# Optimization experiments

Hardware: AMD Instinct MI355X
Metric: run time of the kernel (lower is better)

The kernel has to match this reference:

```python
import jax, jax.numpy as jnp
import numpy as np

B, L1, L2, H = 8, 384, 384, 128


def _lin(k, out_f, in_f, scale=0.05):
    kw, kb = jax.random.split(k)
    return (jax.random.normal(kw, (out_f, in_f), jnp.float32) * scale,
            jax.random.normal(kb, (out_f,), jnp.float32) * scale)


def setup_inputs() -> dict:
    key = jax.random.key(0)
    ks = jax.random.split(key, 10)
    Wq_w, Wq_b = _lin(ks[2], H, H)
    Wup_w, Wup_b = _lin(ks[3], H, H)
    Wvp_w, Wvp_b = _lin(ks[4], H, H)
    V_w, V_b = _lin(ks[5], 1, H)
    Wg_w, Wg_b = _lin(ks[6], 2 * H, 2 * H)
    W_ih, b_ih = _lin(ks[7], 4 * H, 2 * H)
    W_hh, b_hh = _lin(ks[8], 4 * H, H)
    return {
        "x": jax.random.normal(ks[0], (B, L1, H), jnp.float32),
        "x_mask": jnp.zeros((B, L1), dtype=bool),
        "y": jax.random.normal(ks[1], (B, L2, H), jnp.float32),
        "y_mask": jnp.zeros((B, L2), dtype=bool),
        "Wq_w": Wq_w, "Wq_b": Wq_b,
        "Wup_w": Wup_w, "Wup_b": Wup_b,
        "Wvp_w": Wvp_w, "Wvp_b": Wvp_b,
        "V_w": V_w, "V_b": V_b,
        "Wg_w": Wg_w, "Wg_b": Wg_b,
        "W_ih": W_ih, "W_hh": W_hh, "b_ih": b_ih, "b_hh": b_hh,
    }


def reference(x, x_mask, y, y_mask, Wq_w, Wq_b, Wup_w, Wup_b, Wvp_w, Wvp_b,
              V_w, V_b, Wg_w, Wg_b, W_ih, W_hh, b_ih, b_hh):
    b, l1, h = x.shape
    # projections (torch Linear: x @ W.T + b)
    x_proj = x @ Wup_w.T + Wup_b                      # [B, L1, H]
    y_proj = y @ Wq_w.T + Wq_b                        # [B, L2, H]
    # source feeds a constant zero hidden state into W_vp -> just its bias
    hidden_proj = jnp.zeros((h,), x.dtype) @ Wvp_w.T + Wvp_b  # [H]
    # additive attention scores: V . tanh(xp + yp + hp)
    sum_batch = jnp.tanh(x_proj[:, :, None, :] + y_proj[:, None, :, :] + hidden_proj)  # [B,L1,L2,H]
    s = jnp.einsum('btjh,h->btj', sum_batch, V_w[0]) + V_b[0]  # [B, L1, L2]
    # sum_mask = (1 - x_mask) outer (1 - y_mask)
    xm = 1.0 - x_mask.astype(s.dtype)
    ym = 1.0 - y_mask.astype(s.dtype)
    s = s * (xm[:, :, None] * ym[:, None, :])
    s = jnp.where(y_mask[:, None, :], -jnp.inf, s)
    alpha = jax.nn.softmax(s, axis=-1)                # [B, L1, L2]
    ct = jnp.einsum('btj,bjh->bth', alpha, y)         # [B, L1, H]
    merge = jnp.concatenate([x, ct], axis=2)          # [B, L1, 2H]
    gt = jax.nn.sigmoid(merge @ Wg_w.T + Wg_b)
    lstm_in = gt * merge                              # [B, L1, 2H]
    # single-layer unidirectional LSTM (torch gate order: i, f, g, o)
    gates_x = lstm_in @ W_ih.T + b_ih                 # [B, L1, 4H]

    def step(carry, gx):
        h_t, c_t = carry
        g = gx + h_t @ W_hh.T + b_hh
        i, f, gg, o = jnp.split(g, 4, axis=-1)
        c_n = jax.nn.sigmoid(f) * c_t + jax.nn.sigmoid(i) * jnp.tanh(gg)
        h_n = jax.nn.sigmoid(o) * jnp.tanh(c_n)
        return (h_n, c_n), h_n

    init = (jnp.zeros((b, h), x.dtype), jnp.zeros((b, h), x.dtype))
    _, hs = jax.lax.scan(step, init, jnp.swapaxes(gates_x, 0, 1))  # [L1, B, H]
    return jnp.swapaxes(hs, 0, 1)                     # [B, L1, H]
```

## Files before the change

kernel.cpp:

```cpp
#include <hip/hip_runtime.h>
#include <hip/hip_bf16.h>
#include <math.h>

typedef __attribute__((ext_vector_type(4))) float  float4v;
typedef __attribute__((ext_vector_type(2))) float  float2v;
typedef __attribute__((ext_vector_type(8))) short  short8;

#define B_ 8
#define L_ 384
#define H_ 128

__device__ __forceinline__ float bflo(unsigned int u){ unsigned int t = u << 16; float f; __builtin_memcpy(&f,&t,4); return f; }
__device__ __forceinline__ unsigned short f2bf(float f){
  unsigned int t; __builtin_memcpy(&t,&f,4);
  return (unsigned short)((t + 0x7fffu + ((t>>16)&1u)) >> 16);
}
__device__ __forceinline__ float fsig(float x){ return __fdividef(1.f, 1.f + __expf(-x)); }

__device__ __forceinline__ void barrier_lds(){
  asm volatile("s_waitcnt lgkmcnt(0)\n\ts_barrier" ::: "memory");
}

template<int K>
__device__ __forceinline__ void mfma_rowgemm_body(
    unsigned short* in_s,
    const float* __restrict__ inA,
    const float* __restrict__ W, const float* __restrict__ bias,
    const float* __restrict__ bias2, float* __restrict__ out,
    int Ntotal, int act, int row0, int ob)
{
  constexpr int KP = K + 2;
  const int tid  = threadIdx.x;
  const int w    = tid >> 6;
  const int l    = tid & 63;
  const int c    = l & 15;
  const int quad = l >> 4;

  #pragma unroll
  for (int it = 0; it < K/32; ++it) {
    int idx = it*256 + tid;
    int r = idx / (K/4);
    int k = (idx % (K/4)) * 4;
    float4v f = *(const float4v*)(inA + (size_t)(row0+r)*K + k);
    unsigned int p0 = (unsigned int)f2bf(f.x) | ((unsigned int)f2bf(f.y) << 16);
    unsigned int p1 = (unsigned int)f2bf(f.z) | ((unsigned int)f2bf(f.w) << 16);
    *(unsigned int*)&in_s[r*KP + k]     = p0;
    *(unsigned int*)&in_s[r*KP + k + 2] = p1;
  }

  const int n = ob + w*16 + c;
  short8 bfr[K/32];
  #pragma unroll
  for (int kt = 0; kt < K/32; ++kt) {
    const float* src = W + (size_t)n*K + kt*32 + quad*8;
    float4v f0 = *(const float4v*)(src);
    float4v f1 = *(const float4v*)(src + 4);
    short8 v;
    v[0]=(short)f2bf(f0[0]); v[1]=(short)f2bf(f0[1]); v[2]=(short)f2bf(f0[2]); v[3]=(short)f2bf(f0[3]);
    v[4]=(short)f2bf(f1[0]); v[5]=(short)f2bf(f1[1]); v[6]=(short)f2bf(f1[2]); v[7]=(short)f2bf(f1[3]);
    bfr[kt] = v;
  }
  __syncthreads();

  const float4v z4 = {0.f,0.f,0.f,0.f};
  float4v acc0 = z4, acc1 = z4;
  #pragma unroll
  for (int kt = 0; kt < K/32; ++kt) {
    short8 a0 = *(const short8*)&in_s[(c     )*KP + kt*32 + quad*8];
    short8 a1 = *(const short8*)&in_s[(16 + c)*KP + kt*32 + quad*8];
    acc0 = __builtin_amdgcn_mfma_f32_16x16x32_bf16(a0, bfr[kt], acc0, 0,0,0);
    acc1 = __builtin_amdgcn_mfma_f32_16x16x32_bf16(a1, bfr[kt], acc1, 0,0,0);
  }

  const float C2 = 2.8853900817779268f;
  float bv = bias[n] + (bias2 ? bias2[n] : 0.f);
  #pragma unroll
  for (int mt = 0; mt < 2; ++mt) {
    float4v A = mt ? acc1 : acc0;
    #pragma unroll
    for (int r = 0; r < 4; ++r) {
      int m = mt*16 + quad*4 + r;
      float val = A[r] + bv;
      if (act == 4)
        val = __builtin_amdgcn_exp2f(C2 * val);
      if (act == 3)
        out[(size_t)(row0+m)*Ntotal + (n & 127)*4 + (n >> 7)] = val;
      else
        out[(size_t)(row0+m)*Ntotal + n] = val;
    }
  }
}

template<int K>
__global__ __launch_bounds__(256) void mfma_rowgemm_kernel(
    const float* __restrict__ inA,
    const float* __restrict__ W, const float* __restrict__ bias,
    const float* __restrict__ bias2, float* __restrict__ out,
    int Ntotal, int act)
{
  __shared__ __align__(16) unsigned short in_s[32*(K+2)];
  mfma_rowgemm_body<K>(in_s, inA, W, bias, bias2, out,
                       Ntotal, act, blockIdx.x*32, blockIdx.y*64);
}

__global__ __launch_bounds__(256) void proj_mfma_kernel(
    const float* __restrict__ x, const float* __restrict__ y,
    const float* __restrict__ Wup_w, const float* __restrict__ Wup_b,
    const float* __restrict__ Wq_w, const float* __restrict__ Wq_b,
    const float* __restrict__ Wvp_b,
    float* __restrict__ xp, float* __restrict__ yp)
{
  __shared__ __align__(16) unsigned short in_s[32*130];
  int bx = blockIdx.x;
  if (bx < 192)
    mfma_rowgemm_body<128>(in_s, x, Wup_w, Wup_b, nullptr,
                           xp, 128, 4, (bx>>1)*32, (bx&1)*64);
  else {
    bx -= 192;
    mfma_rowgemm_body<128>(in_s, y, Wq_w, Wq_b, Wvp_b,
                           yp, 128, 4, (bx>>1)*32, (bx&1)*64);
  }
}

__global__ __launch_bounds__(256) void attn_kernel(
    const float* __restrict__ xp, const float* __restrict__ yp,
    const float* __restrict__ y, const unsigned char* __restrict__ xmask,
    const unsigned char* __restrict__ ymask, const float* __restrict__ Vw,
    const float* __restrict__ Vb,
    float* __restrict__ ctpbase, float* __restrict__ ml)
{
  __shared__ __align__(16) float xp_s[8][128];
  __shared__ __align__(16) float v2_s[128];
  __shared__ __align__(16) float yp_s[32][132];
  __shared__ __align__(16) unsigned short p_s[16][40];
  __shared__ float sc_s[16];
  __shared__ float xm_s[8];
  __shared__ float ym_s[32];
  __shared__ float sv_s;
  const int tid = threadIdx.x;
  const int b   = blockIdx.y;
  const int t0  = blockIdx.x * 8;
  const int jh  = blockIdx.z;
  const int jb  = jh * 96;
  const int w    = tid >> 6;
  const int l    = tid & 63;
  const int c16  = l & 15;
  const int quad = l >> 4;
  {
    int r = tid >> 5, k4 = (tid & 31) * 4;
    float4v f = *(const float4v*)(xp + ((size_t)(b*L_ + t0 + r))*H_ + k4);
    *(float4v*)&xp_s[r][k4] = f;
    if (tid < 32) {
      float4v v = *(const float4v*)(Vw + tid*4);
      float4v v2; v2[0]=2.f*v[0]; v2[1]=2.f*v[1]; v2[2]=2.f*v[2]; v2[3]=2.f*v[3];
      *(float4v*)&v2_s[tid*4] = v2;
    }
    if (tid < 8) xm_s[tid] = xmask[b*L_ + t0 + tid] ? 0.f : 1.f;
    if (tid < 16) sc_s[tid] = 0.f;
    for (int i = 320 + tid; i < 640; i += 256) ((unsigned short*)p_s)[i] = 0;
  }
  __syncthreads();
  if (tid < 32) {
    float4v v = *(const float4v*)&v2_s[tid*4];
    float sm = (v[0]+v[1]) + (v[2]+v[3]);
    #pragma unroll
    for (int off = 16; off >= 1; off >>= 1) sm += __shfl_xor(sm, off);
    if (tid == 0) sv_s = 0.5f*sm + Vb[0];
  }

  float4v rp[4];
  unsigned char ymb = 0;
  {
    #pragma unroll
    for (int it = 0; it < 4; ++it) {
      int idx = it*256 + tid; int r = idx >> 5; int k4 = (idx & 31) * 4;
      rp[it] = *(const float4v*)(yp + ((size_t)(b*L_ + jb + r))*H_ + k4);
    }
    if (tid < 32) ymb = ymask[b*L_ + jb + tid];
  }

  const int t = tid >> 5, u = tid & 31;
  float mrun = -__builtin_inff(), lrun = 0.f;
  const float4v z4 = {0.f,0.f,0.f,0.f};
  float4v acc0 = z4, acc1 = z4;
  float svc = 0.f, xmv = 0.f;

  for (int c = 0; c < 3; ++c) {
    __syncthreads();
    #pragma unroll
    for (int it = 0; it < 4; ++it) {
      int idx = it*256 + tid; int r = idx >> 5; int k4 = (idx & 31) * 4;
      *(float4v*)&yp_s[r][k4] = rp[it];
    }
    if (tid < 32) ym_s[tid] = ymb ? 0.f : 1.f;
    __syncthreads();
    if (c == 0) { svc = sv_s; xmv = xm_s[t]; }
    short8 yb0, yb1;
    {
      const float* ybase = y + ((size_t)(b*L_ + jb + c*32 + quad*8))*H_ + c16;
      #pragma unroll
      for (int jj = 0; jj < 8; ++jj) {
        yb0[jj] = (short)f2bf(ybase[(size_t)jj*H_ + w*16]);
        yb1[jj] = (short)f2bf(ybase[(size_t)jj*H_ + (w+4)*16]);
      }
    }
    if (c < 2) {
      #pragma unroll
      for (int it = 0; it < 4; ++it) {
        int idx = it*256 + tid; int r = idx >> 5; int k4 = (idx & 31) * 4;
        rp[it] = *(const float4v*)(yp + ((size_t)(b*L_ + jb + (c+1)*32 + r))*H_ + k4);
      }
      if (tid < 32) ymb = ymask[b*L_ + jb + (c+1)*32 + tid];
    }

    float sA = 0.f, sB = 0.f;
    {
      const float* yr = yp_s[u];
      const float* xr = xp_s[t];
      #pragma unroll 4
      for (int k = 0; k < 128; k += 4) {
        float4v yv = *(const float4v*)&yr[k];
        float4v xv = *(const float4v*)&xr[k];
        float4v vv = *(const float4v*)&v2_s[k];
        sA -= vv[0] * __builtin_amdgcn_rcpf(__builtin_fmaf(xv[0], yv[0], 1.f));
        sB -= vv[1] * __builtin_amdgcn_rcpf(__builtin_fmaf(xv[1], yv[1], 1.f));
        sA -= vv[2] * __builtin_amdgcn_rcpf(__builtin_fmaf(xv[2], yv[2], 1.f));
        sB -= vv[3] * __builtin_amdgcn_rcpf(__builtin_fmaf(xv[3], yv[3], 1.f));
      }
    }
    float ymv = ym_s[u];
    float s = (svc + sA + sB) * xmv * ymv;
    if (ymv == 0.f) s = -__builtin_inff();
    float mc = s;
    #pragma unroll
    for (int off = 16; off >= 1; off >>= 1) mc = fmaxf(mc, __shfl_xor(mc, off));
    float mnew = fmaxf(mrun, mc);
    float p  = __expf(s - mnew);
    float sc = __expf(mrun - mnew);
    float ps = p;
    #pragma unroll
    for (int off = 16; off >= 1; off >>= 1) ps += __shfl_xor(ps, off);
    lrun = lrun * sc + ps;
    mrun = mnew;
    p_s[t][u] = f2bf(p);
    if (u == 0) sc_s[t] = sc;
    __syncthreads();
    short8 pf = *(const short8*)&p_s[c16][quad*8];
    float4v scv;
    #pragma unroll
    for (int r = 0; r < 4; ++r) scv[r] = sc_s[quad*4 + r];
    acc0 *= scv; acc1 *= scv;
    acc0 = __builtin_amdgcn_mfma_f32_16x16x32_bf16(pf, yb0, acc0, 0,0,0);
    acc1 = __builtin_amdgcn_mfma_f32_16x16x32_bf16(pf, yb1, acc1, 0,0,0);
  }
  float* ctp = ctpbase + (size_t)jh*393216;
  if (quad < 2) {
    #pragma unroll
    for (int r = 0; r < 4; ++r) {
      int row = b*L_ + t0 + quad*4 + r;
      ctp[(size_t)row*H_ + w*16 + c16]     = acc0[r];
      ctp[(size_t)row*H_ + (w+4)*16 + c16] = acc1[r];
    }
  }
  if (u == 0) {
    int row = b*L_ + t0 + t;
    ml[(jh*2+0)*3072 + row] = mrun;
    ml[(jh*2+1)*3072 + row] = lrun;
  }
}

__global__ __launch_bounds__(256) void gate1_kernel(
    const float* __restrict__ x,
    const float* __restrict__ ctpbase, const float* __restrict__ ml,
    const float* __restrict__ Wg_w, const float* __restrict__ Wg_b,
    float* __restrict__ out)
{
  constexpr int K = 256, KP = 258;
  __shared__ __align__(16) unsigned short in_s[32*KP];
  const int tid  = threadIdx.x;
  const int w    = tid >> 6;
  const int l    = tid & 63;
  const int c    = l & 15;
  const int quad = l >> 4;
  const int row0 = blockIdx.x * 32;
  const int ob   = blockIdx.y * 64;

  #pragma unroll
  for (int it = 0; it < 8; ++it) {
    int idx = it*256 + tid;
    int r = idx >> 6;
    int k = (idx & 63) * 4;
    int row = row0 + r;
    float4v f;
    if (k < 128) {
      f = *(const float4v*)(x + (size_t)row*128 + k);
    } else {
      float m0 = ml[       row], l0 = ml[  3072 + row];
      float m1 = ml[2*3072+row], l1 = ml[3*3072 + row];
      float m2 = ml[4*3072+row], l2 = ml[5*3072 + row];
      float m3 = ml[6*3072+row], l3 = ml[7*3072 + row];
      float mm = fmaxf(fmaxf(m0, m1), fmaxf(m2, m3));
      float e0 = __expf(m0-mm), e1 = __expf(m1-mm);
      float e2 = __expf(m2-mm), e3 = __expf(m3-mm);
      float inv = __fdividef(1.f, (l0*e0 + l1*e1) + (l2*e2 + l3*e3));
      size_t off = (size_t)row*128 + (k-128);
      float4v v0 = *(const float4v*)(ctpbase             + off);
      float4v v1 = *(const float4v*)(ctpbase +   393216  + off);
      float4v v2 = *(const float4v*)(ctpbase + 2*393216  + off);
      float4v v3 = *(const float4v*)(ctpbase + 3*393216  + off);
      f[0] = ((v0[0]*e0 + v1[0]*e1) + (v2[0]*e2 + v3[0]*e3))*inv;
      f[1] = ((v0[1]*e0 + v1[1]*e1) + (v2[1]*e2 + v3[1]*e3))*inv;
      f[2] = ((v0[2]*e0 + v1[2]*e1) + (v2[2]*e2 + v3[2]*e3))*inv;
      f[3] = ((v0[3]*e0 + v1[3]*e1) + (v2[3]*e2 + v3[3]*e3))*inv;
    }
    unsigned int p0 = (unsigned int)f2bf(f[0]) | ((unsigned int)f2bf(f[1]) << 16);
    unsigned int p1 = (unsigned int)f2bf(f[2]) | ((unsigned int)f2bf(f[3]) << 16);
    *(unsigned int*)&in_s[r*KP + k]     = p0;
    *(unsigned int*)&in_s[r*KP + k + 2] = p1;
  }

  const int n = ob + w*16 + c;
  short8 bfr[8];
  #pragma unroll
  for (int kt = 0; kt < 8; ++kt) {
    const float* src = Wg_w + (size_t)n*K + kt*32 + quad*8;
    float4v f0 = *(const float4v*)(src);
    float4v f1 = *(const float4v*)(src + 4);
    short8 v;
    v[0]=(short)f2bf(f0[0]); v[1]=(short)f2bf(f0[1]); v[2]=(short)f2bf(f0[2]); v[3]=(short)f2bf(f0[3]);
    v[4]=(short)f2bf(f1[0]); v[5]=(short)f2bf(f1[1]); v[6]=(short)f2bf(f1[2]); v[7]=(short)f2bf(f1[3]);
    bfr[kt] = v;
  }
  __syncthreads();

  const float4v z4 = {0.f,0.f,0.f,0.f};
  float4v acc0 = z4, acc1 = z4;
  #pragma unroll
  for (int kt = 0; kt < 8; ++kt) {
    short8 a0 = *(const short8*)&in_s[(c     )*KP + kt*32 + quad*8];
    short8 a1 = *(const short8*)&in_s[(16 + c)*KP + kt*32 + quad*8];
    acc0 = __builtin_amdgcn_mfma_f32_16x16x32_bf16(a0, bfr[kt], acc0, 0,0,0);
    acc1 = __builtin_amdgcn_mfma_f32_16x16x32_bf16(a1, bfr[kt], acc1, 0,0,0);
  }

  float bv = Wg_b[n];
  #pragma unroll
  for (int mt = 0; mt < 2; ++mt) {
    float4v A = mt ? acc1 : acc0;
    #pragma unroll
    for (int r = 0; r < 4; ++r) {
      int m = mt*16 + quad*4 + r;
      float val = A[r] + bv;
      float mg = bflo((unsigned int)in_s[m*KP + n]);
      out[(size_t)(row0+m)*256 + n] = fsig(val) * mg;
    }
  }
}

__global__ __launch_bounds__(512) void lstm_kernel(
    const float* __restrict__ gx, const float* __restrict__ Whh,
    float* __restrict__ out)
{
  __shared__ __align__(16) unsigned short h_s[2][128];
  const int tid  = threadIdx.x;
  const int b    = blockIdx.x;
  const int w    = tid >> 6;
  const int l    = tid & 63;
  const int col  = l & 15;
  const int quad = l >> 4;

  short8 bf[4][4];
  #pragma unroll
  for (int nt = 0; nt < 4; ++nt) {
    const int n = nt*128 + w*16 + col;
    #pragma unroll
    for (int kt = 0; kt < 4; ++kt) {
      const int k0 = kt*32 + quad*8;
      const float* src = Whh + (size_t)n*H_ + k0;
      float4v f0 = *(const float4v*)(src);
      float4v f1 = *(const float4v*)(src + 4);
      short8 v;
      v[0]=(short)f2bf(f0[0]); v[1]=(short)f2bf(f0[1]); v[2]=(short)f2bf(f0[2]); v[3]=(short)f2bf(f0[3]);
      v[4]=(short)f2bf(f1[0]); v[5]=(short)f2bf(f1[1]); v[6]=(short)f2bf(f1[2]); v[7]=(short)f2bf(f1[3]);
      bf[nt][kt] = v;
    }
  }

  if (tid < 128) { h_s[0][tid] = 0; h_s[1][tid] = 0; }
  float cst = 0.f;
  const int goff = w*16 + col;
  const float* gbase = gx + (size_t)b*L_*512 + goff*4;
  float* outp = out + (size_t)b*L_*H_ + goff;
  float4v gbuf[4];
  #pragma unroll
  for (int s = 0; s < 4; ++s)
    gbuf[s] = *(const float4v*)(gbase + (size_t)s*512);
  const float4v z4 = {0.f,0.f,0.f,0.f};
  const float NL2E = -1.4426950408889634f;
  const float P2L2E = 2.8853900817779268f;
  __syncthreads();

  for (int t4 = 0; t4 < L_; t4 += 4) {
    #pragma unroll
    for (int s = 0; s < 4; ++s) {
      const int tstep = t4 + s;
      const unsigned short* hb = h_s[s & 1];
      short8 a[4];
      #pragma unroll
      for (int kt=0;kt<4;++kt) a[kt] = *(const short8*)&hb[kt*32 + quad*8];
      float4v c0 = z4, c1 = z4, c2 = z4, c3 = z4;
      #pragma unroll
      for (int kt=0;kt<4;++kt) {
        c0 = __builtin_amdgcn_mfma_f32_16x16x32_bf16(a[kt], bf[0][kt], c0, 0,0,0);
        c1 = __builtin_amdgcn_mfma_f32_16x16x32_bf16(a[kt], bf[1][kt], c1, 0,0,0);
        c2 = __builtin_amdgcn_mfma_f32_16x16x32_bf16(a[kt], bf[2][kt], c2, 0,0,0);
        c3 = __builtin_amdgcn_mfma_f32_16x16x32_bf16(a[kt], bf[3][kt], c3, 0,0,0);
      }
      float g0 = c0[0] + gbuf[s][0];
      float g1 = c1[0] + gbuf[s][1];
      float g2 = c2[0] + gbuf[s][2];
      float g3 = c3[0] + gbuf[s][3];
      if (tstep + 4 < L_)
        gbuf[s] = *(const float4v*)(gbase + (size_t)(tstep+4)*512);
      if (quad == 0) {
        float ig = __builtin_amdgcn_rcpf(1.f + __builtin_amdgcn_exp2f(NL2E*g0));
        float fg = __builtin_amdgcn_rcpf(1.f + __builtin_amdgcn_exp2f(NL2E*g1));
        float gg = 1.f - 2.f*__builtin_amdgcn_rcpf(__builtin_amdgcn_exp2f(P2L2E*g2) + 1.f);
        float og = __builtin_amdgcn_rcpf(1.f + __builtin_amdgcn_exp2f(NL2E*g3));
        cst = fg*cst + ig*gg;
        float hn = og * (1.f - 2.f*__builtin_amdgcn_rcpf(__builtin_amdgcn_exp2f(P2L2E*cst) + 1.f));
        outp[(size_t)tstep*H_] = hn;
        h_s[(s+1)&1][goff] = f2bf(hn);
      }
      barrier_lds();
    }
  }
}

extern "C" void kernel_launch(void* const* d_in, const int* in_sizes, int n_in,
                              void* d_out, int out_size, void* d_ws, size_t ws_size,
                              hipStream_t stream)
{
  (void)in_sizes; (void)n_in; (void)out_size; (void)ws_size;
  const float* x     = (const float*)d_in[0];
  const unsigned char* xm = (const unsigned char*)d_in[1];
  const float* y     = (const float*)d_in[2];
  const unsigned char* ym = (const unsigned char*)d_in[3];
  const float* Wq_w  = (const float*)d_in[4];
  const float* Wq_b  = (const float*)d_in[5];
  const float* Wup_w = (const float*)d_in[6];
  const float* Wup_b = (const float*)d_in[7];
  const float* Wvp_b = (const float*)d_in[9];
  const float* V_w   = (const float*)d_in[10];
  const float* V_b   = (const float*)d_in[11];
  const float* Wg_w  = (const float*)d_in[12];
  const float* Wg_b  = (const float*)d_in[13];
  const float* W_ih  = (const float*)d_in[14];
  const float* W_hh  = (const float*)d_in[15];
  const float* b_ih  = (const float*)d_in[16];
  const float* b_hh  = (const float*)d_in[17];
  float* out = (float*)d_out;

  float* wsf    = (float*)d_ws;
  float* xp_ws  = wsf;
  float* yp_ws  = xp_ws + 393216;
  float* li_ws  = xp_ws;
  float* ctp_ws = yp_ws + 393216;
  float* gx_ws  = ctp_ws + 4*393216;
  float* ml_ws  = gx_ws + 1572864;

  proj_mfma_kernel<<<dim3(384),256,0,stream>>>(x, y, Wup_w, Wup_b, Wq_w, Wq_b, Wvp_b, xp_ws, yp_ws);
  attn_kernel<<<dim3(48,8,4),256,0,stream>>>(xp_ws, yp_ws, y, xm, ym, V_w, V_b, ctp_ws, ml_ws);
  gate1_kernel<<<dim3(96,4),256,0,stream>>>(x, ctp_ws, ml_ws, Wg_w, Wg_b, li_ws);
  mfma_rowgemm_kernel<256><<<dim3(96,8),256,0,stream>>>(li_ws, W_ih, b_ih, b_hh, gx_ws, 512, 3);
  lstm_kernel<<<dim3(8),512,0,stream>>>(gx_ws, W_hh, out);
}
```

Baseline: 331.5 us.

## Replace MFMA LSTM recurrence with per-thread fp16 dot2 rows and shuffles

The LSTM recurrent step no longer uses MFMA tiles where only one quad of lanes does the gate math. Each thread now owns one full row of W_hh, held in registers as 64 fp16 pairs, and computes that gate's dot product with fdot2. The four gates of each hidden unit sit in adjacent lanes, which trade activations with xor shuffles so every lane does useful work. This is meant to cut the per-step latency on the serial critical path, at the cost of heavy register use (128 halves per thread) and fp16 instead of bf16 precision for h and W_hh.

```diff
diff --git a/kernel.cpp b/kernel.cpp
--- a/kernel.cpp
+++ b/kernel.cpp
@@ -5,6 +5,8 @@
 typedef __attribute__((ext_vector_type(4))) float  float4v;
 typedef __attribute__((ext_vector_type(2))) float  float2v;
 typedef __attribute__((ext_vector_type(8))) short  short8;
+typedef __attribute__((ext_vector_type(2))) _Float16 half2v;
+typedef __attribute__((ext_vector_type(8))) _Float16 half8v;
 
 #define B_ 8
 #define L_ 384
@@ -20,6 +22,16 @@
 __device__ __forceinline__ void barrier_lds(){
   asm volatile("s_waitcnt lgkmcnt(0)\n\ts_barrier" ::: "memory");
 }
+
+#if __has_builtin(__builtin_amdgcn_fdot2)
+#define DOT2(a,b,c) __builtin_amdgcn_fdot2((a),(b),(c),false)
+#else
+__device__ __forceinline__ float DOT2f(half2v a, half2v b, float c){
+  return __builtin_fmaf((float)a[0],(float)b[0],
+         __builtin_fmaf((float)a[1],(float)b[1], c));
+}
+#define DOT2(a,b,c) DOT2f((a),(b),(c))
+#endif
 
 template<int K>
 __device__ __forceinline__ void mfma_rowgemm_body(
@@ -361,76 +373,75 @@
     const float* __restrict__ gx, const float* __restrict__ Whh,
     float* __restrict__ out)
 {
-  __shared__ __align__(16) unsigned short h_s[2][128];
-  const int tid  = threadIdx.x;
-  const int b    = blockIdx.x;
-  const int w    = tid >> 6;
-  const int l    = tid & 63;
-  const int col  = l & 15;
-  const int quad = l >> 4;
-
-  short8 bf[4][4];
-  #pragma unroll
-  for (int nt = 0; nt < 4; ++nt) {
-    const int n = nt*128 + w*16 + col;
-    #pragma unroll
-    for (int kt = 0; kt < 4; ++kt) {
-      const int k0 = kt*32 + quad*8;
-      const float* src = Whh + (size_t)n*H_ + k0;
-      float4v f0 = *(const float4v*)(src);
-      float4v f1 = *(const float4v*)(src + 4);
-      short8 v;
-      v[0]=(short)f2bf(f0[0]); v[1]=(short)f2bf(f0[1]); v[2]=(short)f2bf(f0[2]); v[3]=(short)f2bf(f0[3]);
-      v[4]=(short)f2bf(f1[0]); v[5]=(short)f2bf(f1[1]); v[6]=(short)f2bf(f1[2]); v[7]=(short)f2bf(f1[3]);
-      bf[nt][kt] = v;
-    }
-  }
-
-  if (tid < 128) { h_s[0][tid] = 0; h_s[1][tid] = 0; }
+  __shared__ __align__(16) _Float16 h_s[2][128];
+  const int tid = threadIdx.x;
+  const int b   = blockIdx.x;
+  const int d   = tid >> 2;
+  const int g   = tid & 3;
+
+  half2v wt[64];
+  {
+    const float* wrow = Whh + (size_t)(g*128 + d)*H_;
+    #pragma unroll
+    for (int i = 0; i < 32; ++i) {
+      float4v f = *(const float4v*)(wrow + i*4);
+      half2v w0; w0[0] = (_Float16)f[0]; w0[1] = (_Float16)f[1];
+      half2v w1; w1[0] = (_Float16)f[2]; w1[1] = (_Float16)f[3];
+      wt[2*i]   = w0;
+      wt[2*i+1] = w1;
+    }
+  }
+  const float L2E   = 1.4426950408889634f;
+  const float P2L2E = 2.8853900817779268f;
+  const bool  isg   = (g == 2);
+  const float kE = isg ?  P2L2E : -L2E;
+  const float Ac = isg ? -2.f : 1.f;
+  const float Bc = isg ?  1.f : 0.f;
+
+  if (tid < 128) { h_s[0][tid] = (_Float16)0.f; h_s[1][tid] = (_Float16)0.f; }
   float cst = 0.f;
-  const int goff = w*16 + col;
-  const float* gbase = gx + (size_t)b*L_*512 + goff*4;
-  float* outp = out + (size_t)b*L_*H_ + goff;
-  float4v gbuf[4];
-  #pragma unroll
-  for (int s = 0; s < 4; ++s)
-    gbuf[s] = *(const float4v*)(gbase + (size_t)s*512);
-  const float4v z4 = {0.f,0.f,0.f,0.f};
-  const float NL2E = -1.4426950408889634f;
-  const float P2L2E = 2.8853900817779268f;
+  const float* gptr = gx + (size_t)b*L_*512 + tid;
+  float* outp = out + (size_t)b*L_*H_ + d;
+  float gbuf[4];
+  #pragma unroll
+  for (int s = 0; s < 4; ++s) gbuf[s] = gptr[(size_t)s*512];
   __syncthreads();
 
   for (int t4 = 0; t4 < L_; t4 += 4) {
     #pragma unroll
     for (int s = 0; s < 4; ++s) {
       const int tstep = t4 + s;
-      const unsigned short* hb = h_s[s & 1];
-      short8 a[4];
+      const _Float16* hb = h_s[s & 1];
+      float gcur = gbuf[s];
+      if (tstep + 4 < L_)
+        gbuf[s] = gptr[(size_t)(tstep+4)*512];
+      float a0 = 0.f, a1 = 0.f, a2 = 0.f, a3 = 0.f;
       #pragma unroll
-      for (int kt=0;kt<4;++kt) a[kt] = *(const short8*)&hb[kt*32 + quad*8];
-      float4v c0 = z4, c1 = z4, c2 = z4, c3 = z4;
-      #pragma unroll
-      for (int kt=0;kt<4;++kt) {
-        c0 = __builtin_amdgcn_mfma_f32_16x16x32_bf16(a[kt], bf[0][kt], c0, 0,0,0);
-        c1 = __builtin_amdgcn_mfma_f32_16x16x32_bf16(a[kt], bf[1][kt], c1, 0,0,0);
-        c2 = __builtin_amdgcn_mfma_f32_16x16x32_bf16(a[kt], bf[2][kt], c2, 0,0,0);
-        c3 = __builtin_amdgcn_mfma_f32_16x16x32_bf16(a[kt], bf[3][kt], c3, 0,0,0);
+      for (int kt = 0; kt < 16; ++kt) {
+        half8v hv = *(const half8v*)&hb[kt*8];
+        half2v h0; h0[0]=hv[0]; h0[1]=hv[1];
+        half2v h1; h1[0]=hv[2]; h1[1]=hv[3];
+        half2v h2; h2[0]=hv[4]; h2[1]=hv[5];
+        half2v h3; h3[0]=hv[6]; h3[1]=hv[7];
+        a0 = DOT2(h0, wt[kt*4+0], a0);
+        a1 = DOT2(h1, wt[kt*4+1], a1);
+        a2 = DOT2(h2, wt[kt*4+2], a2);
+        a3 = DOT2(h3, wt[kt*4+3], a3);
       }
-      float g0 = c0[0] + gbuf[s][0];
-      float g1 = c1[0] + gbuf[s][1];
-      float g2 = c2[0] + gbuf[s][2];
-      float g3 = c3[0] + gbuf[s][3];
-      if (tstep + 4 < L_)
-        gbuf[s] = *(const float4v*)(gbase + (size_t)(tstep+4)*512);
-      if (quad == 0) {
-        float ig = __builtin_amdgcn_rcpf(1.f + __builtin_amdgcn_exp2f(NL2E*g0));
-        float fg = __builtin_amdgcn_rcpf(1.f + __builtin_amdgcn_exp2f(NL2E*g1));
-        float gg = 1.f - 2.f*__builtin_amdgcn_rcpf(__builtin_amdgcn_exp2f(P2L2E*g2) + 1.f);
-        float og = __builtin_amdgcn_rcpf(1.f + __builtin_amdgcn_exp2f(NL2E*g3));
-        cst = fg*cst + ig*gg;
-        float hn = og * (1.f - 2.f*__builtin_amdgcn_rcpf(__builtin_amdgcn_exp2f(P2L2E*cst) + 1.f));
+      float gate = ((a0 + a1) + (a2 + a3)) + gcur;
+      float e   = __builtin_amdgcn_exp2f(kE * gate);
+      float r   = __builtin_amdgcn_rcpf(1.f + e);
+      float act = __builtin_fmaf(Ac, r, Bc);
+      float xf = __shfl_xor(act, 1);
+      float xg = __shfl_xor(act, 2);
+      float xo = __shfl_xor(xf, 2);
+      cst = __builtin_fmaf(xf, cst, act*xg);
+      float th = 1.f - 2.f*__builtin_amdgcn_rcpf(
+                   __builtin_amdgcn_exp2f(P2L2E*cst) + 1.f);
+      float hn = xo * th;
+      if (g == 0) {
         outp[(size_t)tstep*H_] = hn;
-        h_s[(s+1)&1][goff] = f2bf(hn);
+        h_s[(s+1)&1][d] = (_Float16)hn;
       }
       barrier_lds();
     }
```

Result: slower. 458.6 us (+38.3%).
